# Kernel optimization log

Measured on AMD Instinct MI355X. Metric: run time of the kernel, lower is better.

The kernel has to match this reference:

```python
import jax, jax.numpy as jnp
import numpy as np

B, S, D = 8, 2048, 1024
LN_EPS = 1e-5
N_EPS = 1e-6


def setup_inputs() -> dict:
    key = jax.random.key(0)
    ks = jax.random.split(key, 6)
    s = 1.0 / np.sqrt(D)
    return {
        "x": jax.random.normal(ks[0], (B, S, D), dtype=jnp.float32),
        "W_w": jax.random.uniform(ks[1], (4 * D, D), jnp.float32, -s, s),
        "W_b": jax.random.uniform(ks[2], (4 * D,), jnp.float32, -s, s),
        "U_w": jax.random.uniform(ks[3], (4 * D, D), jnp.float32, -s, s),
        "gamma": jnp.ones((D,), jnp.float32),
        "beta": jnp.zeros((D,), jnp.float32),
    }


def reference(x, W_w, W_b, U_w, gamma, beta):
    # LayerNorm(x)
    mean = jnp.mean(x, axis=-1, keepdims=True)
    var = jnp.mean(jnp.square(x - mean), axis=-1, keepdims=True)
    h_out = (x - mean) * jax.lax.rsqrt(var + LN_EPS) * gamma + beta

    # Precompute input-side projection for all timesteps: (S, B, 4D)
    xW = jnp.einsum('bsd,ed->sbe', h_out, W_w) + W_b

    def step(carry, xw_t):
        h, c, n = carry
        gates = xw_t + h @ U_w.T  # (B, 4D)
        i, f, o, z = jnp.split(gates, 4, axis=-1)
        i_t = jnp.exp(i)
        f_t = jax.nn.sigmoid(f)
        o_t = jax.nn.sigmoid(o)
        c = f_t * c + i_t * jnp.tanh(z)
        n = f_t * n + i_t
        h = o_t * (c / (n + N_EPS))
        return (h, c, n), h

    h0 = jnp.zeros((B, D), x.dtype)
    c0 = jnp.zeros((B, D), x.dtype)
    n0 = jnp.ones((B, D), x.dtype)
    _, ys = jax.lax.scan(step, (h0, c0, n0), xW)  # ys: (S, B, D)
    y = jnp.transpose(ys, (1, 0, 2))
    return x + y
```

## Files before the change

kernel.cpp:

```cpp
#include <hip/hip_runtime.h>
#include <hip/hip_bf16.h>
#include <hip/hip_cooperative_groups.h>

typedef __attribute__((ext_vector_type(8))) short short8;
typedef __attribute__((ext_vector_type(4))) float f32x4;
typedef __attribute__((ext_vector_type(4))) unsigned short ushort4_t;
typedef unsigned long long u64;

#define BB 8
#define SS 2048
#define DD 1024
#define EE 4096
#define NB 64

__device__ __forceinline__ unsigned short f2bf(float f) {
  unsigned int u = __builtin_bit_cast(unsigned int, f);
  u += 0x7fffu + ((u >> 16) & 1u);
  return (unsigned short)(u >> 16);
}
__device__ __forceinline__ float bf2f(unsigned short h) {
  unsigned int u = ((unsigned int)h) << 16;
  return __builtin_bit_cast(float, u);
}

__global__ void cvt2_kernel(const float* __restrict__ Wf, const float* __restrict__ Uf,
                            unsigned short* __restrict__ Wb, unsigned short* __restrict__ Ub) {
  const int n4 = EE * DD / 4;
  for (int i = blockIdx.x * blockDim.x + threadIdx.x; i < n4; i += gridDim.x * blockDim.x) {
    float4 w = ((const float4*)Wf)[i];
    float4 u = ((const float4*)Uf)[i];
    ushort4_t wo, uo;
    wo[0] = f2bf(w.x); wo[1] = f2bf(w.y); wo[2] = f2bf(w.z); wo[3] = f2bf(w.w);
    uo[0] = f2bf(u.x); uo[1] = f2bf(u.y); uo[2] = f2bf(u.z); uo[3] = f2bf(u.w);
    ((ushort4_t*)Wb)[i] = wo;
    ((ushort4_t*)Ub)[i] = uo;
  }
}

__global__ void ln_kernel(const float* __restrict__ x, const float* __restrict__ gamma,
                          const float* __restrict__ beta, unsigned short* __restrict__ hout) {
  int row = blockIdx.x;
  int t = threadIdx.x;
  int wid = t >> 6, lane = t & 63;
  float4 v = ((const float4*)(x + (size_t)row * DD))[t];
  float s = v.x + v.y + v.z + v.w;
  float s2 = v.x * v.x + v.y * v.y + v.z * v.z + v.w * v.w;
  for (int o = 32; o; o >>= 1) { s += __shfl_down(s, o); s2 += __shfl_down(s2, o); }
  __shared__ float rs[4], rq[4];
  if (lane == 0) { rs[wid] = s; rq[wid] = s2; }
  __syncthreads();
  float sum = rs[0] + rs[1] + rs[2] + rs[3];
  float sum2 = rq[0] + rq[1] + rq[2] + rq[3];
  float mean = sum * (1.0f / DD);
  float var = sum2 * (1.0f / DD) - mean * mean;
  float rstd = rsqrtf(var + 1e-5f);
  float4 g = ((const float4*)gamma)[t];
  float4 bt = ((const float4*)beta)[t];
  ushort4_t o4;
  o4[0] = f2bf((v.x - mean) * rstd * g.x + bt.x);
  o4[1] = f2bf((v.y - mean) * rstd * g.y + bt.y);
  o4[2] = f2bf((v.z - mean) * rstd * g.z + bt.z);
  o4[3] = f2bf((v.w - mean) * rstd * g.w + bt.w);
  ((ushort4_t*)(hout + (size_t)row * DD))[t] = o4;
}

__launch_bounds__(256)
__global__ void gemm_xw(const unsigned short* __restrict__ A, const unsigned short* __restrict__ Bm,
                        const float* __restrict__ bias, unsigned short* __restrict__ xw) {
  int rowTile = blockIdx.x;
  int colGrp = blockIdx.y;
  int wid = threadIdx.x >> 6;
  int lane = threadIdx.x & 63;
  int colBase = colGrp * 256 + wid * 64;
  int r0 = rowTile * 64 + (lane & 15);
  int kb = (lane >> 4) * 8;
  f32x4 acc[4][4] = {};
  for (int k0 = 0; k0 < DD; k0 += 32) {
    short8 af[4];
#pragma unroll
    for (int rr = 0; rr < 4; rr++)
      af[rr] = *(const short8*)(A + (size_t)(r0 + rr * 16) * DD + k0 + kb);
#pragma unroll
    for (int c = 0; c < 4; c++) {
      int col = colBase + c * 16 + (lane & 15);
      short8 bf = *(const short8*)(Bm + (size_t)col * DD + k0 + kb);
#pragma unroll
      for (int rr = 0; rr < 4; rr++)
        acc[rr][c] = __builtin_amdgcn_mfma_f32_16x16x32_bf16(af[rr], bf, acc[rr][c], 0, 0, 0);
    }
  }
#pragma unroll
  for (int rr = 0; rr < 4; rr++) {
#pragma unroll
    for (int c = 0; c < 4; c++) {
      int col = colBase + c * 16 + (lane & 15);
      float bv = bias[col];
#pragma unroll
      for (int r2 = 0; r2 < 4; r2++) {
        int R = rowTile * 64 + rr * 16 + (lane >> 4) * 4 + r2;
        int b = R >> 11, sIdx = R & 2047;
        xw[(size_t)sIdx * (BB * EE) + (size_t)b * EE + col] = f2bf(acc[rr][c][r2] + bv);
      }
    }
  }
}

__launch_bounds__(256, 1)
__global__ void scan_kernel(const unsigned short* __restrict__ xw, const unsigned short* __restrict__ Ub,
                            const float* __restrict__ x, float* __restrict__ out,
                            unsigned short* __restrict__ hbuf, int* __restrict__ flags) {
  int bl = blockIdx.x;
  int tid = threadIdx.x;
  int wid = tid >> 6, lane = tid & 63;
  int d0 = bl * 16;

  __shared__ __align__(16) unsigned short h_lds[8 * 1024];
  __shared__ float g_lds[4][8][16];
  __shared__ int ready;
  __shared__ char pad_lds[80 * 1024];
  ((volatile char*)pad_lds)[tid] = 0;
  if (tid == 0) ready = -1;

  int ecol = wid * 1024 + d0 + (lane & 15);
  int kb = (lane >> 4) * 8;
  short8 u[32];
#pragma unroll
  for (int kk = 0; kk < 32; kk++)
    u[kk] = *(const short8*)(Ub + (size_t)ecol * DD + kk * 32 + kb);
#pragma unroll
  for (int kk = 0; kk < 32; kk++)
    asm volatile("" : "+v"(u[kk]));

  float c_s = 0.0f, n_s = 1.0f;
  int ub = tid >> 4, ud = tid & 15;
  bool upd = tid < BB * 16;
  int arow = lane & 7;
  int bq = (lane >> 4) * 4;

  __syncthreads();

  for (int s = 0; s < SS; s++) {
    const unsigned short* xwp = xw + (size_t)s * (BB * EE) + (size_t)wid * 1024 + d0 + (lane & 15);
    unsigned short xv[4] = {0, 0, 0, 0};
    if (bq < BB) {
#pragma unroll
      for (int r2 = 0; r2 < 4; r2++) xv[r2] = xwp[(size_t)(bq + r2) * EE];
    }
    float xin = 0.0f;
    size_t oi = 0;
    if (upd) {
      oi = (size_t)ub * (SS * DD) + (size_t)s * DD + d0 + ud;
      xin = x[oi];
    }

    if (s != 0) {
      if (wid == 0) {
        int f = __hip_atomic_load(flags + lane * 32, __ATOMIC_RELAXED, __HIP_MEMORY_SCOPE_AGENT);
        while (__any(f < s)) {
          f = __hip_atomic_load(flags + lane * 32, __ATOMIC_RELAXED, __HIP_MEMORY_SCOPE_AGENT);
        }
        __hip_atomic_store(&ready, s, __ATOMIC_RELEASE, __HIP_MEMORY_SCOPE_WORKGROUP);
      } else {
        while (__hip_atomic_load(&ready, __ATOMIC_ACQUIRE, __HIP_MEMORY_SCOPE_WORKGROUP) < s) {}
      }
    }

    {
      const u64* hg = (const u64*)(hbuf + (size_t)(s & 1) * (BB * DD));
      u64 tmp[8];
#pragma unroll
      for (int i = 0; i < 8; i++)
        tmp[i] = __hip_atomic_load(hg + tid + i * 256, __ATOMIC_RELAXED, __HIP_MEMORY_SCOPE_AGENT);
#pragma unroll
      for (int i = 0; i < 8; i++) {
        int q = tid + i * 256;
        int row = q >> 8, qoff = q & 255;
        int byte = (row * 2048 + qoff * 8) ^ (row << 4);
        *(u64*)((char*)h_lds + byte) = tmp[i];
      }
    }
    __syncthreads();

    f32x4 a0 = {}, a1 = {}, a2 = {}, a3 = {};
#pragma unroll
    for (int kk = 0; kk < 32; kk += 4) {
      int base = arow * 2048 + (kk * 32 + kb) * 2;
      short8 f0 = *(const short8*)((char*)h_lds + ((base) ^ (arow << 4)));
      short8 f1 = *(const short8*)((char*)h_lds + ((base + 64) ^ (arow << 4)));
      short8 f2 = *(const short8*)((char*)h_lds + ((base + 128) ^ (arow << 4)));
      short8 f3 = *(const short8*)((char*)h_lds + ((base + 192) ^ (arow << 4)));
      a0 = __builtin_amdgcn_mfma_f32_16x16x32_bf16(f0, u[kk], a0, 0, 0, 0);
      a1 = __builtin_amdgcn_mfma_f32_16x16x32_bf16(f1, u[kk + 1], a1, 0, 0, 0);
      a2 = __builtin_amdgcn_mfma_f32_16x16x32_bf16(f2, u[kk + 2], a2, 0, 0, 0);
      a3 = __builtin_amdgcn_mfma_f32_16x16x32_bf16(f3, u[kk + 3], a3, 0, 0, 0);
    }
    f32x4 acc = (a0 + a1) + (a2 + a3);

    if (bq < BB) {
#pragma unroll
      for (int r2 = 0; r2 < 4; r2++)
        g_lds[wid][bq + r2][lane & 15] = acc[r2] + bf2f(xv[r2]);
    }
    __syncthreads();

    float h_val = 0.0f;
    if (upd) {
      float gi = g_lds[0][ub][ud], gf = g_lds[1][ub][ud];
      float go = g_lds[2][ub][ud], gz = g_lds[3][ub][ud];
      float it = __expf(gi);
      float ft = 1.0f / (1.0f + __expf(-gf));
      float ot = 1.0f / (1.0f + __expf(-go));
      float az = fabsf(gz);
      float e2 = __expf(2.0f * az);
      float zt = __builtin_copysignf(1.0f - 2.0f / (e2 + 1.0f), gz);
      c_s = ft * c_s + it * zt;
      n_s = ft * n_s + it;
      h_val = ot * (c_s / (n_s + 1e-6f));
      __hip_atomic_store(hbuf + (size_t)((s + 1) & 1) * (BB * DD) + ub * DD + d0 + ud,
                         f2bf(h_val), __ATOMIC_RELAXED, __HIP_MEMORY_SCOPE_AGENT);
      asm volatile("s_waitcnt vmcnt(0)" ::: "memory");
    }
    __syncthreads();
    if (tid == 0)
      __hip_atomic_store(flags + bl * 32, s + 1, __ATOMIC_RELAXED, __HIP_MEMORY_SCOPE_AGENT);
    if (upd)
      __builtin_nontemporal_store(xin + h_val, out + oi);
  }
}

extern "C" void kernel_launch(void* const* d_in, const int* in_sizes, int n_in,
                              void* d_out, int out_size, void* d_ws, size_t ws_size,
                              hipStream_t stream) {
  const float* xp = (const float*)d_in[0];
  const float* Wwf = (const float*)d_in[1];
  const float* Wbias = (const float*)d_in[2];
  const float* Uwf = (const float*)d_in[3];
  const float* gamma = (const float*)d_in[4];
  const float* beta = (const float*)d_in[5];
  float* outp = (float*)d_out;

  char* w = (char*)d_ws;
  unsigned short* Wb = (unsigned short*)(w);
  unsigned short* Ub = (unsigned short*)(w + 8388608);
  unsigned short* hout = (unsigned short*)(w + 16777216);
  unsigned short* xw = (unsigned short*)(w + 50331648);
  unsigned short* hbuf = (unsigned short*)(w + 184549376);
  int* flags = (int*)(w + 184549376 + 32768);

  hipMemsetAsync((void*)hbuf, 0, 32768 + 8192, stream);

  hipLaunchKernelGGL(cvt2_kernel, dim3(1024), dim3(256), 0, stream, Wwf, Uwf, Wb, Ub);
  hipLaunchKernelGGL(ln_kernel, dim3(BB * SS), dim3(256), 0, stream, xp, gamma, beta, hout);
  hipLaunchKernelGGL(gemm_xw, dim3(256, 16), dim3(256), 0, stream, hout, Wb, Wbias, xw);

  void* args[6];
  const unsigned short* xw_c = xw;
  const unsigned short* ub_c = Ub;
  args[0] = (void*)&xw_c;
  args[1] = (void*)&ub_c;
  args[2] = (void*)&xp;
  args[3] = (void*)&outp;
  args[4] = (void*)&hbuf;
  args[5] = (void*)&flags;
  hipLaunchCooperativeKernel((void*)scan_kernel, dim3(NB), dim3(256), args, 0, stream);
}
```

Measured before the change: 5.755 ms.

## Load recurrent h fragments directly from global memory, dropping LDS staging and barrier

Each wave now polls the cross-block step flags itself instead of having wave 0 poll and signal the others through a shared-memory variable. Each wave then loads its own MFMA A-operand fragments of the previous hidden state straight from the global double buffer, removing the LDS staging copy and one __syncthreads per timestep. The cost is that every wave spins on global flags and reads the full h vector itself, so global/L2 traffic rises roughly fourfold and the fragment loads are uncoalesced 8-byte atomics. The 32 fragment registers also add register pressure next to the 32 resident U fragments.

```diff
diff --git a/kernel.cpp b/kernel.cpp
--- a/kernel.cpp
+++ b/kernel.cpp
@@ -114,12 +114,9 @@
   int wid = tid >> 6, lane = tid & 63;
   int d0 = bl * 16;
 
-  __shared__ __align__(16) unsigned short h_lds[8 * 1024];
   __shared__ float g_lds[4][8][16];
-  __shared__ int ready;
   __shared__ char pad_lds[80 * 1024];
   ((volatile char*)pad_lds)[tid] = 0;
-  if (tid == 0) ready = -1;
 
   int ecol = wid * 1024 + d0 + (lane & 15);
   int kb = (lane >> 4) * 8;
@@ -136,8 +133,7 @@
   bool upd = tid < BB * 16;
   int arow = lane & 7;
   int bq = (lane >> 4) * 4;
-
-  __syncthreads();
+  int qbase = arow * 256 + (lane >> 4) * 2;
 
   for (int s = 0; s < SS; s++) {
     const unsigned short* xwp = xw + (size_t)s * (BB * EE) + (size_t)wid * 1024 + d0 + (lane & 15);
@@ -154,45 +150,34 @@
     }
 
     if (s != 0) {
-      if (wid == 0) {
-        int f = __hip_atomic_load(flags + lane * 32, __ATOMIC_RELAXED, __HIP_MEMORY_SCOPE_AGENT);
-        while (__any(f < s)) {
-          f = __hip_atomic_load(flags + lane * 32, __ATOMIC_RELAXED, __HIP_MEMORY_SCOPE_AGENT);
-        }
-        __hip_atomic_store(&ready, s, __ATOMIC_RELEASE, __HIP_MEMORY_SCOPE_WORKGROUP);
-      } else {
-        while (__hip_atomic_load(&ready, __ATOMIC_ACQUIRE, __HIP_MEMORY_SCOPE_WORKGROUP) < s) {}
+      const int* fp = flags + lane * 32;
+      int f0 = __hip_atomic_load(fp, __ATOMIC_RELAXED, __HIP_MEMORY_SCOPE_AGENT);
+      int f1 = __hip_atomic_load(fp, __ATOMIC_RELAXED, __HIP_MEMORY_SCOPE_AGENT);
+      for (;;) {
+        if (!__any(f0 < s)) break;
+        f0 = f1;
+        f1 = __hip_atomic_load(fp, __ATOMIC_RELAXED, __HIP_MEMORY_SCOPE_AGENT);
       }
     }
-
-    {
-      const u64* hg = (const u64*)(hbuf + (size_t)(s & 1) * (BB * DD));
-      u64 tmp[8];
-#pragma unroll
-      for (int i = 0; i < 8; i++)
-        tmp[i] = __hip_atomic_load(hg + tid + i * 256, __ATOMIC_RELAXED, __HIP_MEMORY_SCOPE_AGENT);
-#pragma unroll
-      for (int i = 0; i < 8; i++) {
-        int q = tid + i * 256;
-        int row = q >> 8, qoff = q & 255;
-        int byte = (row * 2048 + qoff * 8) ^ (row << 4);
-        *(u64*)((char*)h_lds + byte) = tmp[i];
-      }
-    }
-    __syncthreads();
+    asm volatile("" ::: "memory");
+
+    const u64* hb = (const u64*)hbuf + (size_t)(s & 1) * 2048;
+    short8 fr[32];
+#pragma unroll
+    for (int kk = 0; kk < 32; kk++) {
+      union { u64 q[2]; short8 v; } cvt;
+      cvt.q[0] = __hip_atomic_load(hb + qbase + kk * 8, __ATOMIC_RELAXED, __HIP_MEMORY_SCOPE_AGENT);
+      cvt.q[1] = __hip_atomic_load(hb + qbase + kk * 8 + 1, __ATOMIC_RELAXED, __HIP_MEMORY_SCOPE_AGENT);
+      fr[kk] = cvt.v;
+    }
 
     f32x4 a0 = {}, a1 = {}, a2 = {}, a3 = {};
 #pragma unroll
     for (int kk = 0; kk < 32; kk += 4) {
-      int base = arow * 2048 + (kk * 32 + kb) * 2;
-      short8 f0 = *(const short8*)((char*)h_lds + ((base) ^ (arow << 4)));
-      short8 f1 = *(const short8*)((char*)h_lds + ((base + 64) ^ (arow << 4)));
-      short8 f2 = *(const short8*)((char*)h_lds + ((base + 128) ^ (arow << 4)));
-      short8 f3 = *(const short8*)((char*)h_lds + ((base + 192) ^ (arow << 4)));
-      a0 = __builtin_amdgcn_mfma_f32_16x16x32_bf16(f0, u[kk], a0, 0, 0, 0);
-      a1 = __builtin_amdgcn_mfma_f32_16x16x32_bf16(f1, u[kk + 1], a1, 0, 0, 0);
-      a2 = __builtin_amdgcn_mfma_f32_16x16x32_bf16(f2, u[kk + 2], a2, 0, 0, 0);
-      a3 = __builtin_amdgcn_mfma_f32_16x16x32_bf16(f3, u[kk + 3], a3, 0, 0, 0);
+      a0 = __builtin_amdgcn_mfma_f32_16x16x32_bf16(fr[kk + 0], u[kk + 0], a0, 0, 0, 0);
+      a1 = __builtin_amdgcn_mfma_f32_16x16x32_bf16(fr[kk + 1], u[kk + 1], a1, 0, 0, 0);
+      a2 = __builtin_amdgcn_mfma_f32_16x16x32_bf16(fr[kk + 2], u[kk + 2], a2, 0, 0, 0);
+      a3 = __builtin_amdgcn_mfma_f32_16x16x32_bf16(fr[kk + 3], u[kk + 3], a3, 0, 0, 0);
     }
     f32x4 acc = (a0 + a1) + (a2 + a3);
 
```

Measured after the change: 20.25 ms. +251.9%, slower.

## Poll flags from every wave, load h as dwords, apply gate activations per wave

Applied to the files above, without the earlier changes.

Every wave now spins on the cross-block flags itself, replacing the scheme where wave 0 polled and then released the other waves through an LDS ready flag. The initial block barrier goes away along with that flag. The h broadcast load switches from 8 64-bit atomic loads to 16 32-bit loads per thread, and the LDS swizzle is recomputed to match. Gate nonlinearities now run in the MFMA-owning wave before the results are written to LDS, which spreads the transcendental work across all four waves instead of 128 update threads. The trade is four times the global flag polling traffic and twice as many load instructions for h.

```diff
diff --git a/kernel.cpp b/kernel.cpp
--- a/kernel.cpp
+++ b/kernel.cpp
@@ -5,7 +5,6 @@
 typedef __attribute__((ext_vector_type(8))) short short8;
 typedef __attribute__((ext_vector_type(4))) float f32x4;
 typedef __attribute__((ext_vector_type(4))) unsigned short ushort4_t;
-typedef unsigned long long u64;
 
 #define BB 8
 #define SS 2048
@@ -116,10 +115,8 @@
 
   __shared__ __align__(16) unsigned short h_lds[8 * 1024];
   __shared__ float g_lds[4][8][16];
-  __shared__ int ready;
   __shared__ char pad_lds[80 * 1024];
   ((volatile char*)pad_lds)[tid] = 0;
-  if (tid == 0) ready = -1;
 
   int ecol = wid * 1024 + d0 + (lane & 15);
   int kb = (lane >> 4) * 8;
@@ -137,8 +134,6 @@
   int arow = lane & 7;
   int bq = (lane >> 4) * 4;
 
-  __syncthreads();
-
   for (int s = 0; s < SS; s++) {
     const unsigned short* xwp = xw + (size_t)s * (BB * EE) + (size_t)wid * 1024 + d0 + (lane & 15);
     unsigned short xv[4] = {0, 0, 0, 0};
@@ -154,29 +149,24 @@
     }
 
     if (s != 0) {
-      if (wid == 0) {
-        int f = __hip_atomic_load(flags + lane * 32, __ATOMIC_RELAXED, __HIP_MEMORY_SCOPE_AGENT);
-        while (__any(f < s)) {
-          f = __hip_atomic_load(flags + lane * 32, __ATOMIC_RELAXED, __HIP_MEMORY_SCOPE_AGENT);
-        }
-        __hip_atomic_store(&ready, s, __ATOMIC_RELEASE, __HIP_MEMORY_SCOPE_WORKGROUP);
-      } else {
-        while (__hip_atomic_load(&ready, __ATOMIC_ACQUIRE, __HIP_MEMORY_SCOPE_WORKGROUP) < s) {}
+      int f = __hip_atomic_load(flags + lane * 32, __ATOMIC_RELAXED, __HIP_MEMORY_SCOPE_AGENT);
+      while (__any(f < s)) {
+        f = __hip_atomic_load(flags + lane * 32, __ATOMIC_RELAXED, __HIP_MEMORY_SCOPE_AGENT);
       }
     }
 
     {
-      const u64* hg = (const u64*)(hbuf + (size_t)(s & 1) * (BB * DD));
-      u64 tmp[8];
-#pragma unroll
-      for (int i = 0; i < 8; i++)
+      const unsigned int* hg = (const unsigned int*)(hbuf + (size_t)(s & 1) * (BB * DD));
+      unsigned int tmp[16];
+#pragma unroll
+      for (int i = 0; i < 16; i++)
         tmp[i] = __hip_atomic_load(hg + tid + i * 256, __ATOMIC_RELAXED, __HIP_MEMORY_SCOPE_AGENT);
 #pragma unroll
-      for (int i = 0; i < 8; i++) {
-        int q = tid + i * 256;
-        int row = q >> 8, qoff = q & 255;
-        int byte = (row * 2048 + qoff * 8) ^ (row << 4);
-        *(u64*)((char*)h_lds + byte) = tmp[i];
+      for (int i = 0; i < 16; i++) {
+        int dw = tid + i * 256;
+        int row = dw >> 9;
+        int byte = (row * 2048 + (dw & 511) * 4) ^ (row << 4);
+        *(unsigned int*)((char*)h_lds + byte) = tmp[i];
       }
     }
     __syncthreads();
@@ -198,21 +188,27 @@
 
     if (bq < BB) {
 #pragma unroll
-      for (int r2 = 0; r2 < 4; r2++)
-        g_lds[wid][bq + r2][lane & 15] = acc[r2] + bf2f(xv[r2]);
+      for (int r2 = 0; r2 < 4; r2++) {
+        float v = acc[r2] + bf2f(xv[r2]);
+        float t;
+        if (wid == 0) {
+          t = __expf(v);
+        } else if (wid == 3) {
+          float az = fabsf(v);
+          float e2 = __expf(2.0f * az);
+          t = __builtin_copysignf(1.0f - 2.0f / (e2 + 1.0f), v);
+        } else {
+          t = 1.0f / (1.0f + __expf(-v));
+        }
+        g_lds[wid][bq + r2][lane & 15] = t;
+      }
     }
     __syncthreads();
 
     float h_val = 0.0f;
     if (upd) {
-      float gi = g_lds[0][ub][ud], gf = g_lds[1][ub][ud];
-      float go = g_lds[2][ub][ud], gz = g_lds[3][ub][ud];
-      float it = __expf(gi);
-      float ft = 1.0f / (1.0f + __expf(-gf));
-      float ot = 1.0f / (1.0f + __expf(-go));
-      float az = fabsf(gz);
-      float e2 = __expf(2.0f * az);
-      float zt = __builtin_copysignf(1.0f - 2.0f / (e2 + 1.0f), gz);
+      float it = g_lds[0][ub][ud], ft = g_lds[1][ub][ud];
+      float ot = g_lds[2][ub][ud], zt = g_lds[3][ub][ud];
       c_s = ft * c_s + it * zt;
       n_s = ft * n_s + it;
       h_val = ot * (c_s / (n_s + 1e-6f));
```

After: 6.067 ms. +5.4%, slower.
